# Kernel tuning notes

Measured on AMD Instinct MI355X. Metric: run time of the kernel, lower is better.

The kernel has to match this reference:

```python
import jax, jax.numpy as jnp
import numpy as np

LN_EPS = 1e-5


def layer_norm(x, g, b):
    m = jnp.mean(x, axis=-1, keepdims=True)
    v = jnp.mean((x - m) ** 2, axis=-1, keepdims=True)
    return (x - m) * jax.lax.rsqrt(v + LN_EPS) * g + b


def sppcf(x):
    # x: [B, de], de = 4*d. Multi-scale avg-pool + strided interleave assembly.
    B, de = x.shape
    d = de // 4
    p2 = x.reshape(B, de // 2, 2).mean(-1)          # kernel=2, stride=2 -> [B, 2d]
    p4 = x.reshape(B, d, 4).mean(-1)                # kernel=4, stride=4 -> [B, d]
    # kernel=16, stride=4 pooling via cumsum: out[i] = mean(x[:, 4i:4i+16]), i in [0, d-4]
    cs = jnp.concatenate([jnp.zeros((B, 1), x.dtype), jnp.cumsum(x, axis=1)], axis=1)
    starts = jnp.arange(d - 3) * 4
    p16 = (cs[:, starts + 16] - cs[:, starts]) / 16.0  # [B, d-3]
    # fused_output2[:, :-3] = p16 ; fused_output2[:, -3:] = fused_output2[:, -7:-4] = p16[:, -4:-1]
    f2 = jnp.concatenate([p16, p16[:, -4:-1]], axis=1)  # [B, d]
    # out[0::2]=p2, out[1::4]=p4, out[3::4]=f2  <=>  interleave groups of 4
    out = jnp.stack([p2[:, 0::2], p4, p2[:, 1::2], f2], axis=-1).reshape(B, de)
    return out


def setup_inputs() -> dict:
    key = jax.random.key(0)
    ks = jax.random.split(key, 8)
    B, S, C = 16384, 25, 200
    E, D, H, NC = 2, 4 * C, 32, 16  # encoder_n, dim, mlp_dim, num_classes
    inp = {
        "x": jax.random.normal(ks[0], (B, S, C), dtype=jnp.float32),
        "lnA_g": jnp.ones((E, D), jnp.float32),
        "lnA_b": jnp.zeros((E, D), jnp.float32),
        "lnB_g": jnp.ones((E, D), jnp.float32),
        "lnB_b": jnp.zeros((E, D), jnp.float32),
        "w1": jax.random.normal(ks[1], (E, D, H), jnp.float32) * (1.0 / np.sqrt(D)),
        "b1": jnp.zeros((E, H), jnp.float32),
        "w2": jax.random.normal(ks[2], (E, H, D), jnp.float32) * (1.0 / np.sqrt(H)),
        "b2": jnp.zeros((E, D), jnp.float32),
        "fc_w": jax.random.normal(ks[3], (C, NC), jnp.float32) * (1.0 / np.sqrt(C)),
        "fc_b": jnp.zeros((NC,), jnp.float32),
    }
    return inp


def reference(x, lnA_g, lnA_b, lnB_g, lnB_b, w1, b1, w2, b2, fc_w, fc_b):
    B, S, C = x.shape
    E = lnA_g.shape[0]
    # CFModule.cross_fuse: interleave min/mean/last/max over spectral-neighbor axis
    body = x[:, :-1, :]
    h = jnp.stack(
        [body.min(axis=1), body.mean(axis=1), x[:, -1, :], body.max(axis=1)], axis=-1
    ).reshape(B, 4 * C)
    for i in range(E):
        # Residual(PreNorm(SPPCFModule))
        h = h + sppcf(layer_norm(h, lnA_g[i], lnA_b[i]))
        # Residual(PreNorm(FeedForward))  (dropout=0 -> identity)
        z = layer_norm(h, lnB_g[i], lnB_b[i])
        z = jax.nn.gelu(z @ w1[i] + b1[i], approximate=False) @ w2[i] + b2[i]
        h = h + z
    # n_pool=1, channels % 1 == 0 branch: view [B, C, 4].mean then fc0
    pooled = h.reshape(B, C, 4).mean(axis=-1)
    return pooled @ fc_w + fc_b
```

## Files before the change

kernel.cpp:

```cpp
#include <hip/hip_runtime.h>
#include <math.h>

namespace {

constexpr int kC  = 200;
constexpr int kD  = 800;
constexpr int kS  = 25;
constexpr int kH  = 32;
constexpr int kNC = 16;
constexpr int kR  = 4;
constexpr int kRW = 800;

typedef float vfloat4 __attribute__((ext_vector_type(4)));

__device__ __forceinline__ int woff(int m) { return (m << 2) ^ ((m & 0x38) >> 1); }

__device__ __forceinline__ float4 ld4(const float* p) { return *(const float4*)p; }
__device__ __forceinline__ float4 ld4nt(const float* p) {
    vfloat4 v = __builtin_nontemporal_load((const vfloat4*)p);
    return make_float4(v.x, v.y, v.z, v.w);
}
__device__ __forceinline__ void   st4(float* p, float4 v) { *(float4*)p = v; }
__device__ __forceinline__ float  hsum4(float4 v) { return (v.x + v.y) + (v.z + v.w); }

__device__ __forceinline__ float4 f4fma(float s, float4 w, float4 a) {
    a.x = fmaf(s, w.x, a.x); a.y = fmaf(s, w.y, a.y);
    a.z = fmaf(s, w.z, a.z); a.w = fmaf(s, w.w, a.w);
    return a;
}

__device__ __forceinline__ void wfence() {
    asm volatile("s_waitcnt lgkmcnt(0)" ::: "memory");
}

__global__ __launch_bounds__(256)
void featurize_kernel(const float* __restrict__ x, float* __restrict__ hws, int Btot)
{
    const int gid = blockIdx.x * 256 + threadIdx.x;
    if (gid >= Btot * 50) return;
    const int row = gid / 50;
    const int cq  = gid - row * 50;

    const float* xp = x + (size_t)row * (kS * kC) + cq * 4;
    float4 v = ld4nt(xp);
    float4 mn = v, mx = v, sm = v;
    #pragma unroll
    for (int s = 1; s < kS - 1; ++s) {
        float4 u = ld4nt(xp + s * kC);
        mn.x = fminf(mn.x, u.x); mx.x = fmaxf(mx.x, u.x); sm.x += u.x;
        mn.y = fminf(mn.y, u.y); mx.y = fmaxf(mx.y, u.y); sm.y += u.y;
        mn.z = fminf(mn.z, u.z); mx.z = fmaxf(mx.z, u.z); sm.z += u.z;
        mn.w = fminf(mn.w, u.w); mx.w = fmaxf(mx.w, u.w); sm.w += u.w;
    }
    float4 last = ld4nt(xp + (kS - 1) * kC);
    const float i24 = 1.0f / 24.0f;
    float* hp = hws + (size_t)row * kD + 16 * cq;
    st4(hp + 0,  make_float4(mn.x, sm.x * i24, last.x, mx.x));
    st4(hp + 4,  make_float4(mn.y, sm.y * i24, last.y, mx.y));
    st4(hp + 8,  make_float4(mn.z, sm.z * i24, last.z, mx.z));
    st4(hp + 12, make_float4(mn.w, sm.w * i24, last.w, mx.w));
}

__device__ __forceinline__ void ln_row(const float* hrow, float* yrow,
                                       const float* __restrict__ g,
                                       const float* __restrict__ bb, int j)
{
    const bool tail = (j < 8);
    float4 v0 = ld4(&hrow[woff(j)]);
    float4 v1 = ld4(&hrow[woff(j + 64)]);
    float4 v2 = ld4(&hrow[woff(j + 128)]);
    float4 v3 = make_float4(0.f, 0.f, 0.f, 0.f);
    if (tail) v3 = ld4(&hrow[woff(192 + j)]);

    float sm = hsum4(v0) + hsum4(v1) + hsum4(v2) + hsum4(v3);
    #pragma unroll
    for (int mk = 32; mk >= 1; mk >>= 1) sm += __shfl_xor(sm, mk, 64);
    const float mean = sm * (1.0f / 800.0f);

    float ssq = 0.f;
    { float a=v0.x-mean,b=v0.y-mean,c=v0.z-mean,d=v0.w-mean; ssq += a*a+b*b+c*c+d*d; }
    { float a=v1.x-mean,b=v1.y-mean,c=v1.z-mean,d=v1.w-mean; ssq += a*a+b*b+c*c+d*d; }
    { float a=v2.x-mean,b=v2.y-mean,c=v2.z-mean,d=v2.w-mean; ssq += a*a+b*b+c*c+d*d; }
    if (tail) { float a=v3.x-mean,b=v3.y-mean,c=v3.z-mean,d=v3.w-mean; ssq += a*a+b*b+c*c+d*d; }
    #pragma unroll
    for (int mk = 32; mk >= 1; mk >>= 1) ssq += __shfl_xor(ssq, mk, 64);
    const float rstd = rsqrtf(ssq * (1.0f / 800.0f) + 1e-5f);

    auto stc = [&](int m, float4 v) {
        float4 g4 = ld4(&g[4 * m]);
        float4 b4 = ld4(&bb[4 * m]);
        float4 y;
        y.x = (v.x - mean) * rstd * g4.x + b4.x;
        y.y = (v.y - mean) * rstd * g4.y + b4.y;
        y.z = (v.z - mean) * rstd * g4.z + b4.z;
        y.w = (v.w - mean) * rstd * g4.w + b4.w;
        st4(&yrow[woff(m)], y);
    };
    stc(j, v0); stc(j + 64, v1); stc(j + 128, v2);
    if (tail) stc(192 + j, v3);
}

__device__ __forceinline__ void sppcf_add(const float* yrow, float* hrow, int j)
{
    auto one = [&](int m) {
        const int kk = (m <= 196) ? m : m - 4;
        float4 q0 = ld4(&yrow[woff(kk)]);
        float4 q1 = ld4(&yrow[woff(kk + 1)]);
        float4 q2 = ld4(&yrow[woff(kk + 2)]);
        float4 q3 = ld4(&yrow[woff(kk + 3)]);
        float4 y4 = (m <= 196) ? q0 : ld4(&yrow[woff(m)]);
        const float s16 = hsum4(q0) + hsum4(q1) + hsum4(q2) + hsum4(q3);
        float4 h4 = ld4(&hrow[woff(m)]);
        h4.x += (y4.x + y4.y) * 0.5f;
        h4.y += (y4.x + y4.y + y4.z + y4.w) * 0.25f;
        h4.z += (y4.z + y4.w) * 0.5f;
        h4.w += s16 * (1.0f / 16.0f);
        st4(&hrow[woff(m)], h4);
    };
    one(j); one(j + 64); one(j + 128);
    if (j < 8) one(192 + j);
}

template<bool FROMWS>
__global__ __launch_bounds__(256)
void essp_main(const float* __restrict__ src,
               const float* __restrict__ lnA_g, const float* __restrict__ lnA_b,
               const float* __restrict__ lnB_g, const float* __restrict__ lnB_b,
               const float* __restrict__ w1, const float* __restrict__ b1,
               const float* __restrict__ w2, const float* __restrict__ b2,
               const float* __restrict__ fc_w, const float* __restrict__ fc_b,
               float* __restrict__ out, int Btot)
{
    __shared__ float hs[kR * kRW];
    __shared__ float zb[kR * kRW];
    __shared__ float vb[kR * kH];

    const int t   = threadIdx.x;
    const int w   = t >> 6;
    const int j   = t & 63;
    const int b0  = blockIdx.x * kR;
    const int row = b0 + w;

    if constexpr (FROMWS) {
        if (row < Btot) {
            const float* hg = src + (size_t)row * kD;
            float* hr = &hs[w * kRW];
            st4(&hr[woff(j)],       ld4(&hg[4 * j]));
            st4(&hr[woff(j + 64)],  ld4(&hg[4 * (j + 64)]));
            st4(&hr[woff(j + 128)], ld4(&hg[4 * (j + 128)]));
            if (j < 8) st4(&hr[woff(192 + j)], ld4(&hg[4 * (192 + j)]));
        }
    } else {
        if (j < 50 && row < Btot) {
            const float* xp = src + (size_t)row * (kS * kC) + j * 4;
            float4 v = ld4nt(xp);
            float4 mn = v, mx = v, sm = v;
            #pragma unroll
            for (int s = 1; s < kS - 1; ++s) {
                float4 u = ld4nt(xp + s * kC);
                mn.x = fminf(mn.x, u.x); mx.x = fmaxf(mx.x, u.x); sm.x += u.x;
                mn.y = fminf(mn.y, u.y); mx.y = fmaxf(mx.y, u.y); sm.y += u.y;
                mn.z = fminf(mn.z, u.z); mx.z = fmaxf(mx.z, u.z); sm.z += u.z;
                mn.w = fminf(mn.w, u.w); mx.w = fmaxf(mx.w, u.w); sm.w += u.w;
            }
            float4 last = ld4nt(xp + (kS - 1) * kC);
            const float i24 = 1.0f / 24.0f;
            float* hr = &hs[w * kRW];
            st4(&hr[woff(4 * j + 0)], make_float4(mn.x, sm.x * i24, last.x, mx.x));
            st4(&hr[woff(4 * j + 1)], make_float4(mn.y, sm.y * i24, last.y, mx.y));
            st4(&hr[woff(4 * j + 2)], make_float4(mn.z, sm.z * i24, last.z, mx.z));
            st4(&hr[woff(4 * j + 3)], make_float4(mn.w, sm.w * i24, last.w, mx.w));
        }
    }
    wfence();

    for (int layer = 0; layer < 2; ++layer) {
        const float* gA  = lnA_g + layer * kD;
        const float* bAv = lnA_b + layer * kD;
        const float* gB  = lnB_g + layer * kD;
        const float* bBv = lnB_b + layer * kD;
        const float* w1p = w1 + layer * kD * kH;
        const float* b1p = b1 + layer * kH;
        const float* w2p = w2 + layer * kH * kD;
        const float* b2p = b2 + layer * kD;

        ln_row(&hs[w * kRW], &zb[w * kRW], gA, bAv, j);
        wfence();
        sppcf_add(&zb[w * kRW], &hs[w * kRW], j);
        wfence();
        ln_row(&hs[w * kRW], &zb[w * kRW], gB, bBv, j);
        __syncthreads();

        float4 acc0 = make_float4(0,0,0,0), acc1 = acc0, acc2 = acc0, acc3 = acc0;
        const int dg = t >> 3, cg = t & 7;
        if (t < 200) {
            #pragma unroll
            for (int cc = 0; cc < 8; ++cc) {
                const int m = dg * 8 + cc, d0 = 4 * m;
                float4 wr0 = ld4(&w1p[(d0 + 0) * kH + 4 * cg]);
                float4 wr1 = ld4(&w1p[(d0 + 1) * kH + 4 * cg]);
                float4 wr2 = ld4(&w1p[(d0 + 2) * kH + 4 * cg]);
                float4 wr3 = ld4(&w1p[(d0 + 3) * kH + 4 * cg]);
                float4 z0 = ld4(&zb[0 * kRW + woff(m)]);
                float4 z1 = ld4(&zb[1 * kRW + woff(m)]);
                float4 z2 = ld4(&zb[2 * kRW + woff(m)]);
                float4 z3 = ld4(&zb[3 * kRW + woff(m)]);
                acc0 = f4fma(z0.x, wr0, acc0); acc0 = f4fma(z0.y, wr1, acc0);
                acc0 = f4fma(z0.z, wr2, acc0); acc0 = f4fma(z0.w, wr3, acc0);
                acc1 = f4fma(z1.x, wr0, acc1); acc1 = f4fma(z1.y, wr1, acc1);
                acc1 = f4fma(z1.z, wr2, acc1); acc1 = f4fma(z1.w, wr3, acc1);
                acc2 = f4fma(z2.x, wr0, acc2); acc2 = f4fma(z2.y, wr1, acc2);
                acc2 = f4fma(z2.z, wr2, acc2); acc2 = f4fma(z2.w, wr3, acc2);
                acc3 = f4fma(z3.x, wr0, acc3); acc3 = f4fma(z3.y, wr1, acc3);
                acc3 = f4fma(z3.z, wr2, acc3); acc3 = f4fma(z3.w, wr3, acc3);
            }
        }
        __syncthreads();
        if (t < 200) {
            const int pb = dg * 32 + ((4 * cg) ^ ((dg & 7) << 2));
            st4(&zb[0 * kRW + pb], acc0);
            st4(&zb[1 * kRW + pb], acc1);
            st4(&zb[2 * kRW + pb], acc2);
            st4(&zb[3 * kRW + pb], acc3);
        }
        __syncthreads();

        if (t < 128) {
            const int r = t >> 5, h = t & 31;
            float u = b1p[h];
            #pragma unroll
            for (int dq = 0; dq < 25; ++dq)
                u += zb[r * kRW + dq * 32 + (h ^ ((dq & 7) << 2))];
            vb[r * kH + h] = 0.5f * u * (1.0f + erff(u * 0.70710678118654752440f));
        }
        __syncthreads();

        if (t < 200) {
            float4 a0 = make_float4(0,0,0,0), a1 = a0, a2 = a0, a3 = a0;
            #pragma unroll
            for (int hc = 0; hc < 8; ++hc) {
                float4 wq0 = ld4(&w2p[(4*hc + 0) * kD + 4*t]);
                float4 wq1 = ld4(&w2p[(4*hc + 1) * kD + 4*t]);
                float4 wq2 = ld4(&w2p[(4*hc + 2) * kD + 4*t]);
                float4 wq3 = ld4(&w2p[(4*hc + 3) * kD + 4*t]);
                float4 vq;
                vq = ld4(&vb[0 * kH + 4*hc]);
                a0 = f4fma(vq.x, wq0, a0); a0 = f4fma(vq.y, wq1, a0);
                a0 = f4fma(vq.z, wq2, a0); a0 = f4fma(vq.w, wq3, a0);
                vq = ld4(&vb[1 * kH + 4*hc]);
                a1 = f4fma(vq.x, wq0, a1); a1 = f4fma(vq.y, wq1, a1);
                a1 = f4fma(vq.z, wq2, a1); a1 = f4fma(vq.w, wq3, a1);
                vq = ld4(&vb[2 * kH + 4*hc]);
                a2 = f4fma(vq.x, wq0, a2); a2 = f4fma(vq.y, wq1, a2);
                a2 = f4fma(vq.z, wq2, a2); a2 = f4fma(vq.w, wq3, a2);
                vq = ld4(&vb[3 * kH + 4*hc]);
                a3 = f4fma(vq.x, wq0, a3); a3 = f4fma(vq.y, wq1, a3);
                a3 = f4fma(vq.z, wq2, a3); a3 = f4fma(vq.w, wq3, a3);
            }
            const float4 bq = ld4(&b2p[4*t]);
            const int wo = woff(t);
            { float4 h4 = ld4(&hs[0*kRW + wo]);
              h4.x += a0.x+bq.x; h4.y += a0.y+bq.y; h4.z += a0.z+bq.z; h4.w += a0.w+bq.w;
              st4(&hs[0*kRW + wo], h4); }
            { float4 h4 = ld4(&hs[1*kRW + wo]);
              h4.x += a1.x+bq.x; h4.y += a1.y+bq.y; h4.z += a1.z+bq.z; h4.w += a1.w+bq.w;
              st4(&hs[1*kRW + wo], h4); }
            { float4 h4 = ld4(&hs[2*kRW + wo]);
              h4.x += a2.x+bq.x; h4.y += a2.y+bq.y; h4.z += a2.z+bq.z; h4.w += a2.w+bq.w;
              st4(&hs[2*kRW + wo], h4); }
            { float4 h4 = ld4(&hs[3*kRW + wo]);
              h4.x += a3.x+bq.x; h4.y += a3.y+bq.y; h4.z += a3.z+bq.z; h4.w += a3.w+bq.w;
              st4(&hs[3*kRW + wo], h4); }
        }
        __syncthreads();
    }

    {
        const float* hr = &hs[w * kRW];
        float* pr = &zb[w * kRW];
        pr[j]       = hsum4(ld4(&hr[woff(j)]))       * 0.25f;
        pr[j + 64]  = hsum4(ld4(&hr[woff(j + 64)]))  * 0.25f;
        pr[j + 128] = hsum4(ld4(&hr[woff(j + 128)])) * 0.25f;
        if (j < 8) pr[192 + j] = hsum4(ld4(&hr[woff(192 + j)])) * 0.25f;
    }
    wfence();

    {
        const int n = j & 15, sg = j >> 4;
        const float* pr = &zb[w * kRW + sg * 50];
        const float* fw = fc_w + (size_t)(sg * 50) * kNC + n;
        float acc = 0.f;
        #pragma unroll 10
        for (int i = 0; i < 50; ++i) acc += pr[i] * fw[i * kNC];
        acc += __shfl_xor(acc, 16, 64);
        acc += __shfl_xor(acc, 32, 64);
        if (j < kNC && row < Btot)
            out[(size_t)row * kNC + j] = acc + fc_b[j];
    }
}

}

extern "C" void kernel_launch(void* const* d_in, const int* in_sizes, int n_in,
                              void* d_out, int out_size, void* d_ws, size_t ws_size,
                              hipStream_t stream) {
    const float* x     = (const float*)d_in[0];
    const float* lnA_g = (const float*)d_in[1];
    const float* lnA_b = (const float*)d_in[2];
    const float* lnB_g = (const float*)d_in[3];
    const float* lnB_b = (const float*)d_in[4];
    const float* w1    = (const float*)d_in[5];
    const float* b1    = (const float*)d_in[6];
    const float* w2    = (const float*)d_in[7];
    const float* b2    = (const float*)d_in[8];
    const float* fc_w  = (const float*)d_in[9];
    const float* fc_b  = (const float*)d_in[10];
    float* out = (float*)d_out;

    const int Btot   = in_sizes[0] / (kS * kC);
    const int blocks = (Btot + kR - 1) / kR;
    const size_t hbytes = (size_t)Btot * kD * sizeof(float);

    if (ws_size >= hbytes) {
        float* hws = (float*)d_ws;
        const int fblocks = (Btot * 50 + 255) / 256;
        hipLaunchKernelGGL(featurize_kernel, dim3(fblocks), dim3(256), 0, stream,
                           x, hws, Btot);
        hipLaunchKernelGGL((essp_main<true>), dim3(blocks), dim3(256), 0, stream,
                           hws, lnA_g, lnA_b, lnB_g, lnB_b, w1, b1, w2, b2,
                           fc_w, fc_b, out, Btot);
    } else {
        hipLaunchKernelGGL((essp_main<false>), dim3(blocks), dim3(256), 0, stream,
                           x, lnA_g, lnA_b, lnB_g, lnB_b, w1, b1, w2, b2,
                           fc_w, fc_b, out, Btot);
    }
}
```

Measured before the change: 220.2 us.

## Process eight rows per block to amortize weight loads across more rows

Doubles the rows per 256-thread block from four to eight, so each wave handles two rows in the input reduction, layernorm, SPPCF and final FC stages. The MLP matmuls now reuse each loaded w1/w2 vector across eight rows instead of four, halving weight traffic per row. In exchange, shared memory per block doubles (about 51 KB), which lowers occupancy, and register pressure rises from the eight float4 accumulators.

```diff
diff --git a/kernel.cpp b/kernel.cpp
--- a/kernel.cpp
+++ b/kernel.cpp
@@ -8,7 +8,7 @@
 constexpr int kS  = 25;
 constexpr int kH  = 32;
 constexpr int kNC = 16;
-constexpr int kR  = 4;
+constexpr int kR  = 8;
 constexpr int kRW = 800;
 
 typedef float vfloat4 __attribute__((ext_vector_type(4)));
@@ -139,37 +139,41 @@
     const int w   = t >> 6;
     const int j   = t & 63;
     const int b0  = blockIdx.x * kR;
-    const int row = b0 + w;
-
-    if constexpr (FROMWS) {
-        if (row < Btot) {
-            const float* hg = src + (size_t)row * kD;
-            float* hr = &hs[w * kRW];
-            st4(&hr[woff(j)],       ld4(&hg[4 * j]));
-            st4(&hr[woff(j + 64)],  ld4(&hg[4 * (j + 64)]));
-            st4(&hr[woff(j + 128)], ld4(&hg[4 * (j + 128)]));
-            if (j < 8) st4(&hr[woff(192 + j)], ld4(&hg[4 * (192 + j)]));
-        }
-    } else {
-        if (j < 50 && row < Btot) {
-            const float* xp = src + (size_t)row * (kS * kC) + j * 4;
-            float4 v = ld4nt(xp);
-            float4 mn = v, mx = v, sm = v;
-            #pragma unroll
-            for (int s = 1; s < kS - 1; ++s) {
-                float4 u = ld4nt(xp + s * kC);
-                mn.x = fminf(mn.x, u.x); mx.x = fmaxf(mx.x, u.x); sm.x += u.x;
-                mn.y = fminf(mn.y, u.y); mx.y = fmaxf(mx.y, u.y); sm.y += u.y;
-                mn.z = fminf(mn.z, u.z); mx.z = fmaxf(mx.z, u.z); sm.z += u.z;
-                mn.w = fminf(mn.w, u.w); mx.w = fmaxf(mx.w, u.w); sm.w += u.w;
-            }
-            float4 last = ld4nt(xp + (kS - 1) * kC);
-            const float i24 = 1.0f / 24.0f;
-            float* hr = &hs[w * kRW];
-            st4(&hr[woff(4 * j + 0)], make_float4(mn.x, sm.x * i24, last.x, mx.x));
-            st4(&hr[woff(4 * j + 1)], make_float4(mn.y, sm.y * i24, last.y, mx.y));
-            st4(&hr[woff(4 * j + 2)], make_float4(mn.z, sm.z * i24, last.z, mx.z));
-            st4(&hr[woff(4 * j + 3)], make_float4(mn.w, sm.w * i24, last.w, mx.w));
+
+    #pragma unroll
+    for (int rr = 0; rr < 2; ++rr) {
+        const int lr  = w + 4 * rr;
+        const int row = b0 + lr;
+        if constexpr (FROMWS) {
+            if (row < Btot) {
+                const float* hg = src + (size_t)row * kD;
+                float* hr = &hs[lr * kRW];
+                st4(&hr[woff(j)],       ld4(&hg[4 * j]));
+                st4(&hr[woff(j + 64)],  ld4(&hg[4 * (j + 64)]));
+                st4(&hr[woff(j + 128)], ld4(&hg[4 * (j + 128)]));
+                if (j < 8) st4(&hr[woff(192 + j)], ld4(&hg[4 * (192 + j)]));
+            }
+        } else {
+            if (j < 50 && row < Btot) {
+                const float* xp = src + (size_t)row * (kS * kC) + j * 4;
+                float4 v = ld4nt(xp);
+                float4 mn = v, mx = v, sm = v;
+                #pragma unroll
+                for (int s = 1; s < kS - 1; ++s) {
+                    float4 u = ld4nt(xp + s * kC);
+                    mn.x = fminf(mn.x, u.x); mx.x = fmaxf(mx.x, u.x); sm.x += u.x;
+                    mn.y = fminf(mn.y, u.y); mx.y = fmaxf(mx.y, u.y); sm.y += u.y;
+                    mn.z = fminf(mn.z, u.z); mx.z = fmaxf(mx.z, u.z); sm.z += u.z;
+                    mn.w = fminf(mn.w, u.w); mx.w = fmaxf(mx.w, u.w); sm.w += u.w;
+                }
+                float4 last = ld4nt(xp + (kS - 1) * kC);
+                const float i24 = 1.0f / 24.0f;
+                float* hr = &hs[lr * kRW];
+                st4(&hr[woff(4 * j + 0)], make_float4(mn.x, sm.x * i24, last.x, mx.x));
+                st4(&hr[woff(4 * j + 1)], make_float4(mn.y, sm.y * i24, last.y, mx.y));
+                st4(&hr[woff(4 * j + 2)], make_float4(mn.z, sm.z * i24, last.z, mx.z));
+                st4(&hr[woff(4 * j + 3)], make_float4(mn.w, sm.w * i24, last.w, mx.w));
+            }
         }
     }
     wfence();
@@ -185,14 +189,19 @@
         const float* b2p = b2 + layer * kD;
 
         ln_row(&hs[w * kRW], &zb[w * kRW], gA, bAv, j);
+        ln_row(&hs[(w + 4) * kRW], &zb[(w + 4) * kRW], gA, bAv, j);
         wfence();
         sppcf_add(&zb[w * kRW], &hs[w * kRW], j);
+        sppcf_add(&zb[(w + 4) * kRW], &hs[(w + 4) * kRW], j);
         wfence();
         ln_row(&hs[w * kRW], &zb[w * kRW], gB, bBv, j);
-        __syncthreads();
-
-        float4 acc0 = make_float4(0,0,0,0), acc1 = acc0, acc2 = acc0, acc3 = acc0;
+        ln_row(&hs[(w + 4) * kRW], &zb[(w + 4) * kRW], gB, bBv, j);
+        __syncthreads();
+
+        float4 acc[kR];
         const int dg = t >> 3, cg = t & 7;
+        #pragma unroll
+        for (int r = 0; r < kR; ++r) acc[r] = make_float4(0.f, 0.f, 0.f, 0.f);
         if (t < 200) {
             #pragma unroll
             for (int cc = 0; cc < 8; ++cc) {
@@ -201,31 +210,26 @@
                 float4 wr1 = ld4(&w1p[(d0 + 1) * kH + 4 * cg]);
                 float4 wr2 = ld4(&w1p[(d0 + 2) * kH + 4 * cg]);
                 float4 wr3 = ld4(&w1p[(d0 + 3) * kH + 4 * cg]);
-                float4 z0 = ld4(&zb[0 * kRW + woff(m)]);
-                float4 z1 = ld4(&zb[1 * kRW + woff(m)]);
-                float4 z2 = ld4(&zb[2 * kRW + woff(m)]);
-                float4 z3 = ld4(&zb[3 * kRW + woff(m)]);
-                acc0 = f4fma(z0.x, wr0, acc0); acc0 = f4fma(z0.y, wr1, acc0);
-                acc0 = f4fma(z0.z, wr2, acc0); acc0 = f4fma(z0.w, wr3, acc0);
-                acc1 = f4fma(z1.x, wr0, acc1); acc1 = f4fma(z1.y, wr1, acc1);
-                acc1 = f4fma(z1.z, wr2, acc1); acc1 = f4fma(z1.w, wr3, acc1);
-                acc2 = f4fma(z2.x, wr0, acc2); acc2 = f4fma(z2.y, wr1, acc2);
-                acc2 = f4fma(z2.z, wr2, acc2); acc2 = f4fma(z2.w, wr3, acc2);
-                acc3 = f4fma(z3.x, wr0, acc3); acc3 = f4fma(z3.y, wr1, acc3);
-                acc3 = f4fma(z3.z, wr2, acc3); acc3 = f4fma(z3.w, wr3, acc3);
+                const int wo = woff(m);
+                #pragma unroll
+                for (int r = 0; r < kR; ++r) {
+                    float4 z = ld4(&zb[r * kRW + wo]);
+                    acc[r] = f4fma(z.x, wr0, acc[r]);
+                    acc[r] = f4fma(z.y, wr1, acc[r]);
+                    acc[r] = f4fma(z.z, wr2, acc[r]);
+                    acc[r] = f4fma(z.w, wr3, acc[r]);
+                }
             }
         }
         __syncthreads();
         if (t < 200) {
             const int pb = dg * 32 + ((4 * cg) ^ ((dg & 7) << 2));
-            st4(&zb[0 * kRW + pb], acc0);
-            st4(&zb[1 * kRW + pb], acc1);
-            st4(&zb[2 * kRW + pb], acc2);
-            st4(&zb[3 * kRW + pb], acc3);
-        }
-        __syncthreads();
-
-        if (t < 128) {
+            #pragma unroll
+            for (int r = 0; r < kR; ++r) st4(&zb[r * kRW + pb], acc[r]);
+        }
+        __syncthreads();
+
+        {
             const int r = t >> 5, h = t & 31;
             float u = b1p[h];
             #pragma unroll
@@ -236,48 +240,42 @@
         __syncthreads();
 
         if (t < 200) {
-            float4 a0 = make_float4(0,0,0,0), a1 = a0, a2 = a0, a3 = a0;
+            float4 a2[kR];
+            #pragma unroll
+            for (int r = 0; r < kR; ++r) a2[r] = make_float4(0.f, 0.f, 0.f, 0.f);
             #pragma unroll
             for (int hc = 0; hc < 8; ++hc) {
                 float4 wq0 = ld4(&w2p[(4*hc + 0) * kD + 4*t]);
                 float4 wq1 = ld4(&w2p[(4*hc + 1) * kD + 4*t]);
                 float4 wq2 = ld4(&w2p[(4*hc + 2) * kD + 4*t]);
                 float4 wq3 = ld4(&w2p[(4*hc + 3) * kD + 4*t]);
-                float4 vq;
-                vq = ld4(&vb[0 * kH + 4*hc]);
-                a0 = f4fma(vq.x, wq0, a0); a0 = f4fma(vq.y, wq1, a0);
-                a0 = f4fma(vq.z, wq2, a0); a0 = f4fma(vq.w, wq3, a0);
-                vq = ld4(&vb[1 * kH + 4*hc]);
-                a1 = f4fma(vq.x, wq0, a1); a1 = f4fma(vq.y, wq1, a1);
-                a1 = f4fma(vq.z, wq2, a1); a1 = f4fma(vq.w, wq3, a1);
-                vq = ld4(&vb[2 * kH + 4*hc]);
-                a2 = f4fma(vq.x, wq0, a2); a2 = f4fma(vq.y, wq1, a2);
-                a2 = f4fma(vq.z, wq2, a2); a2 = f4fma(vq.w, wq3, a2);
-                vq = ld4(&vb[3 * kH + 4*hc]);
-                a3 = f4fma(vq.x, wq0, a3); a3 = f4fma(vq.y, wq1, a3);
-                a3 = f4fma(vq.z, wq2, a3); a3 = f4fma(vq.w, wq3, a3);
+                #pragma unroll
+                for (int r = 0; r < kR; ++r) {
+                    float4 vq = ld4(&vb[r * kH + 4*hc]);
+                    a2[r] = f4fma(vq.x, wq0, a2[r]);
+                    a2[r] = f4fma(vq.y, wq1, a2[r]);
+                    a2[r] = f4fma(vq.z, wq2, a2[r]);
+                    a2[r] = f4fma(vq.w, wq3, a2[r]);
+                }
             }
             const float4 bq = ld4(&b2p[4*t]);
             const int wo = woff(t);
-            { float4 h4 = ld4(&hs[0*kRW + wo]);
-              h4.x += a0.x+bq.x; h4.y += a0.y+bq.y; h4.z += a0.z+bq.z; h4.w += a0.w+bq.w;
-              st4(&hs[0*kRW + wo], h4); }
-            { float4 h4 = ld4(&hs[1*kRW + wo]);
-              h4.x += a1.x+bq.x; h4.y += a1.y+bq.y; h4.z += a1.z+bq.z; h4.w += a1.w+bq.w;
-              st4(&hs[1*kRW + wo], h4); }
-            { float4 h4 = ld4(&hs[2*kRW + wo]);
-              h4.x += a2.x+bq.x; h4.y += a2.y+bq.y; h4.z += a2.z+bq.z; h4.w += a2.w+bq.w;
-              st4(&hs[2*kRW + wo], h4); }
-            { float4 h4 = ld4(&hs[3*kRW + wo]);
-              h4.x += a3.x+bq.x; h4.y += a3.y+bq.y; h4.z += a3.z+bq.z; h4.w += a3.w+bq.w;
-              st4(&hs[3*kRW + wo], h4); }
-        }
-        __syncthreads();
-    }
-
-    {
-        const float* hr = &hs[w * kRW];
-        float* pr = &zb[w * kRW];
+            #pragma unroll
+            for (int r = 0; r < kR; ++r) {
+                float4 h4 = ld4(&hs[r * kRW + wo]);
+                h4.x += a2[r].x + bq.x; h4.y += a2[r].y + bq.y;
+                h4.z += a2[r].z + bq.z; h4.w += a2[r].w + bq.w;
+                st4(&hs[r * kRW + wo], h4);
+            }
+        }
+        __syncthreads();
+    }
+
+    #pragma unroll
+    for (int rr = 0; rr < 2; ++rr) {
+        const int lr = w + 4 * rr;
+        const float* hr = &hs[lr * kRW];
+        float* pr = &zb[lr * kRW];
         pr[j]       = hsum4(ld4(&hr[woff(j)]))       * 0.25f;
         pr[j + 64]  = hsum4(ld4(&hr[woff(j + 64)]))  * 0.25f;
         pr[j + 128] = hsum4(ld4(&hr[woff(j + 128)])) * 0.25f;
@@ -285,9 +283,12 @@
     }
     wfence();
 
-    {
+    #pragma unroll
+    for (int rr = 0; rr < 2; ++rr) {
+        const int lr  = w + 4 * rr;
+        const int row = b0 + lr;
         const int n = j & 15, sg = j >> 4;
-        const float* pr = &zb[w * kRW + sg * 50];
+        const float* pr = &zb[lr * kRW + sg * 50];
         const float* fw = fc_w + (size_t)(sg * 50) * kNC + n;
         float acc = 0.f;
         #pragma unroll 10
```

Measured after the change: 190.6 us (median of 3 runs). -13.5%, faster.
